# Kernel optimization log

Hardware: AMD Instinct MI355X
Metric: run time of the kernel (lower is better)

Reference implementation:

```python
import jax, jax.numpy as jnp
from jax import lax
import numpy as np

DIM = 384
HEADS = 8
B, H, W = 8, 128, 128
_DN = ('NCHW', 'OIHW', 'NCHW')


def setup_inputs() -> dict:
    key = jax.random.key(0)
    ks = jax.random.split(key, 8)
    x = jax.random.normal(ks[0], (B, DIM, H, W), jnp.float32)
    qkv_w = jax.random.normal(ks[1], (3 * DIM, DIM, 1, 1), jnp.float32) * 0.02
    qkv_b = jax.random.normal(ks[2], (3 * DIM,), jnp.float32) * 0.02
    dw_w = jax.random.normal(ks[3], (3 * DIM, 1, 3, 3), jnp.float32) * 0.02
    dw_b = jax.random.normal(ks[4], (3 * DIM,), jnp.float32) * 0.02
    proj_w = jax.random.normal(ks[5], (DIM, DIM, 1, 1), jnp.float32) * 0.02
    proj_b = jax.random.normal(ks[6], (DIM,), jnp.float32) * 0.02
    temperature = jnp.ones((HEADS, 1, 1), jnp.float32)
    return {"x": x, "qkv_w": qkv_w, "qkv_b": qkv_b, "dw_w": dw_w,
            "dw_b": dw_b, "proj_w": proj_w, "proj_b": proj_b,
            "temperature": temperature}


def _l2norm(t, eps=1e-12):
    # F.normalize(t, dim=-1): divide by max(||t||_2, eps)
    n = jnp.sqrt(jnp.sum(t * t, axis=-1, keepdims=True))
    return t / jnp.maximum(n, eps)


def reference(x, qkv_w, qkv_b, dw_w, dw_b, proj_w, proj_b, temperature):
    b, C, h, w = x.shape
    heads = HEADS
    c = C // heads
    hw = h * w
    # 1x1 pointwise qkv conv
    qkv = lax.conv_general_dilated(x, qkv_w, (1, 1), 'VALID',
                                   dimension_numbers=_DN) + qkv_b[None, :, None, None]
    # 3x3 depthwise conv, padding=1
    qkv = lax.conv_general_dilated(qkv, dw_w, (1, 1), ((1, 1), (1, 1)),
                                   feature_group_count=3 * C,
                                   dimension_numbers=_DN) + dw_b[None, :, None, None]
    q, k, v = jnp.split(qkv, 3, axis=1)
    # b (head c) h w -> b head c (h w)
    q = q.reshape(b, heads, c, hw)
    k = k.reshape(b, heads, c, hw)
    v = v.reshape(b, heads, c, hw)
    q = _l2norm(q)
    k = _l2norm(k)
    # processor scales q by temperature*sqrt(hw); SDPA divides by sqrt(hw):
    # net logits = temperature * q_n @ k_n^T  (CxC channel attention per head)
    temp = temperature.reshape(1, heads, 1, 1)
    logits = jnp.einsum('bhcn,bhdn->bhcd', q * temp, k)
    attn = jax.nn.softmax(logits, axis=-1)
    out = jnp.einsum('bhcd,bhdn->bhcn', attn, v)  # [b, heads, c, hw]
    out = out.reshape(b, C, h, w)
    return lax.conv_general_dilated(out, proj_w, (1, 1), 'VALID',
                                    dimension_numbers=_DN) + proj_b[None, :, None, None]
```

## Files before the change

### kernel.cpp

```cpp
#include <hip/hip_runtime.h>
#include <hip/hip_bf16.h>
#include <cstdint>


#define BATCH 8
#define DIM 384
#define HEADS 8
#define CH 48
#define HW 16384
#define C3 1152
#define MPAD1 1280
#define WPAD 512

typedef __attribute__((ext_vector_type(8))) short bf16x8;
typedef __attribute__((ext_vector_type(8))) unsigned short u16x8;
typedef __attribute__((ext_vector_type(4))) float f32x4;

__device__ __forceinline__ float b2f(ushort b) {
  union { float f; unsigned u; } x; x.u = ((unsigned)b) << 16; return x.f;
}
__device__ __forceinline__ ushort f2b(float f) {
  union { float f; unsigned u; } x; x.f = f;
  unsigned r = x.u + 0x7fffu + ((x.u >> 16) & 1u);
  return (ushort)(r >> 16);
}

__device__ __forceinline__ void async16(const ushort* g, ushort* l) {
  __builtin_amdgcn_global_load_lds(
      (const __attribute__((address_space(1))) unsigned int*)(unsigned long long)(uintptr_t)g,
      (__attribute__((address_space(3))) unsigned int*)(unsigned int)(uintptr_t)l,
      16, 0, 0);
}

__global__ __launch_bounds__(256) void cast_w(const float* __restrict__ s,
                                              ushort* __restrict__ d, int n) {
  int i = (blockIdx.x * 256 + threadIdx.x) * 4;
  if (i + 3 < n) {
    float4 v = *(const float4*)(s + i);
    ushort4 o = make_ushort4(f2b(v.x), f2b(v.y), f2b(v.z), f2b(v.w));
    *(ushort4*)(d + i) = o;
  }
}

template <typename SrcT, int OUT_BF16>
__global__ __launch_bounds__(512, 1) void gemm_px2(
    const ushort* __restrict__ A, const SrcT* __restrict__ src,
    const float* __restrict__ bias, void* __restrict__ Cout,
    int Mpad, int Mreal, long Asb, long Ssb, long Csb) {
  constexpr int K = DIM;
  int zb = blockIdx.y;
  int px0 = blockIdx.x * 128;
  const ushort* Ab = A + (size_t)zb * Asb;
  const SrcT* Sb = src + (size_t)zb * Ssb;
  __shared__ __align__(16) ushort Bs[128 * 384];
  __shared__ __align__(16) ushort As[2][256 * 64];
  int tid = threadIdx.x, lane = tid & 63, wid = tid >> 6;
  int wm = wid >> 1, wn = wid & 1;
  int fr = lane & 15, fs = lane >> 4;

  {
    int pix = tid & 127;
    int cg = tid >> 7;
#pragma unroll
    for (int rr = 0; rr < 12; ++rr) {
      int c8 = cg + rr * 4;
      u16x8 pk;
#pragma unroll
      for (int j = 0; j < 8; ++j) {
        int c = c8 * 8 + j;
        if constexpr (sizeof(SrcT) == 4)
          pk[j] = f2b(((const float*)Sb)[(size_t)c * HW + px0 + pix]);
        else
          pk[j] = ((const ushort*)Sb)[(size_t)c * HW + px0 + pix];
      }
      *(u16x8*)&Bs[pix * 384 + ((c8 ^ (pix & 7)) << 3)] = pk;
    }
  }

  auto stageA = [&](int buf, int mt, int k0) {
#pragma unroll
    for (int q = 0; q < 4; ++q) {
      int r = q * 64 + wid * 8 + (lane >> 3);
      int col = ((lane & 7) ^ (r & 7)) * 8;
      async16(Ab + (size_t)(mt * 256 + r) * K + k0 + col,
              &As[buf][(q * 64 + wid * 8) * 64]);
    }
  };

  f32x4 acc[4][4];
  auto compute = [&](int buf, int t) {
#pragma unroll
    for (int kk = 0; kk < 2; ++kk) {
      bf16x8 af[4], bv[4];
#pragma unroll
      for (int m = 0; m < 4; ++m) {
        int R = wm * 64 + m * 16 + fr;
        int slot = kk * 4 + fs;
        af[m] = *(const bf16x8*)&As[buf][R * 64 + ((slot ^ (R & 7)) << 3)];
      }
#pragma unroll
      for (int n = 0; n < 4; ++n) {
        int P = wn * 64 + n * 16 + fr;
        int gslot = t * 8 + kk * 4 + fs;
        bv[n] = *(const bf16x8*)&Bs[P * 384 + ((gslot ^ (P & 7)) << 3)];
      }
#pragma unroll
      for (int m = 0; m < 4; ++m)
#pragma unroll
        for (int n = 0; n < 4; ++n)
          acc[m][n] = __builtin_amdgcn_mfma_f32_16x16x32_bf16(af[m], bv[n], acc[m][n], 0, 0, 0);
    }
  };

  const int MT = Mpad >> 8;
  const int TOT = MT * 6;
  __syncthreads();
  stageA(0, 0, 0);
  stageA(1, 0, 64);
  int nmt = 0, nt = 2;

  for (int mt = 0; mt < MT; ++mt) {
    f32x4 zero = {0.f, 0.f, 0.f, 0.f};
#pragma unroll
    for (int m = 0; m < 4; ++m)
#pragma unroll
      for (int n = 0; n < 4; ++n) acc[m][n] = zero;
#pragma unroll
    for (int t = 0; t < 6; ++t) {
      int idx = mt * 6 + t;
      if (idx + 1 < TOT) {
        asm volatile("s_waitcnt vmcnt(4)" ::: "memory");
      } else {
        asm volatile("s_waitcnt vmcnt(0)" ::: "memory");
      }
      __builtin_amdgcn_s_barrier();
      asm volatile("" ::: "memory");
      __builtin_amdgcn_sched_barrier(0);
      __builtin_amdgcn_s_setprio(1);
      compute(idx & 1, t);
      __builtin_amdgcn_s_setprio(0);
      __builtin_amdgcn_sched_barrier(0);
      asm volatile("" ::: "memory");
      __builtin_amdgcn_s_barrier();
      if (idx + 2 < TOT) {
        stageA(idx & 1, nmt, nt * 64);
        if (++nt == 6) { nt = 0; ++nmt; }
      }
    }
#pragma unroll
    for (int m = 0; m < 4; ++m)
#pragma unroll
      for (int j = 0; j < 4; ++j) {
        int gr = mt * 256 + wm * 64 + m * 16 + fs * 4 + j;
        if (gr < Mreal) {
          float bz = bias[gr];
#pragma unroll
          for (int n = 0; n < 4; ++n) {
            int gc = px0 + wn * 64 + n * 16 + fr;
            float v = acc[m][n][j] + bz;
            if constexpr (OUT_BF16)
              ((ushort*)Cout)[(size_t)zb * Csb + (size_t)gr * HW + gc] = f2b(v);
            else
              ((float*)Cout)[(size_t)zb * Csb + (size_t)gr * HW + gc] = v;
          }
        }
      }
  }
}

__global__ __launch_bounds__(256) void dwconv(
    const ushort* __restrict__ in, const float* __restrict__ w9,
    const float* __restrict__ b9, ushort* __restrict__ out,
    float* __restrict__ sq) {
  int ch = blockIdx.x;
  int b = blockIdx.y;
  const size_t plane = ((size_t)b * C3 + ch) * HW;
  int tid = threadIdx.x, lane = tid & 63;
  int rg = tid >> 4, cg = tid & 15;
  int r0 = rg * 8, c0 = cg * 8;

  float w[9];
#pragma unroll
  for (int i = 0; i < 9; ++i) w[i] = w9[ch * 9 + i];
  float bias = b9[ch];

  float a0[8], a1[8];
#pragma unroll
  for (int c = 0; c < 8; ++c) { a0[c] = 0.f; a1[c] = 0.f; }
  float ss = 0.f;

#pragma unroll
  for (int it = 0; it < 10; ++it) {
    int r = r0 - 1 + it;
    float x[8];
    if ((unsigned)r < 128u) {
      u16x8 raw = *(const u16x8*)(in + plane + (size_t)r * 128 + c0);
#pragma unroll
      for (int c = 0; c < 8; ++c) x[c] = b2f(raw[c]);
    } else {
#pragma unroll
      for (int c = 0; c < 8; ++c) x[c] = 0.f;
    }
    float xl = __shfl(x[7], lane - 1);
    float xr = __shfl(x[0], lane + 1);
    if (cg == 0) xl = 0.f;
    if (cg == 15) xr = 0.f;

    float h0[8], h1[8], h2[8];
#pragma unroll
    for (int c = 0; c < 8; ++c) {
      float l = (c == 0) ? xl : x[c - 1];
      float rt = (c == 7) ? xr : x[c + 1];
      h0[c] = w[0] * l + w[1] * x[c] + w[2] * rt;
      h1[c] = w[3] * l + w[4] * x[c] + w[5] * rt;
      h2[c] = w[6] * l + w[7] * x[c] + w[8] * rt;
    }
    if (it >= 2) {
      int R = r - 1;
      u16x8 pk;
#pragma unroll
      for (int c = 0; c < 8; ++c) {
        float o = a0[c] + h2[c] + bias;
        ss += o * o;
        pk[c] = f2b(o);
      }
      *(u16x8*)(out + plane + (size_t)R * 128 + c0) = pk;
    }
#pragma unroll
    for (int c = 0; c < 8; ++c) { a0[c] = a1[c] + h1[c]; a1[c] = h0[c]; }
  }

  if (ch < 2 * DIM) {
#pragma unroll
    for (int off = 32; off; off >>= 1) ss += __shfl_down(ss, off, 64);
    if (lane == 0) atomicAdd(&sq[b * 2 * DIM + ch], ss);
  }
}

__global__ __launch_bounds__(256) void gram(const ushort* __restrict__ qkvd,
                                            float* __restrict__ G) {
  int chunk = blockIdx.x;
  int bh = blockIdx.y;
  int b = bh >> 3, h = bh & 7;
  int tid = threadIdx.x, lane = tid & 63, wid = tid >> 6;
  const ushort* qbase = qkvd + ((size_t)b * C3 + h * CH) * HW;
  const ushort* kbase = qbase + (size_t)DIM * HW;
  int pix0 = chunk * 1024 + wid * 256;
  int fr = lane & 15, fk = (lane >> 4) * 8;
  f32x4 zero = {0.f, 0.f, 0.f, 0.f};
  f32x4 acc[3][3];
#pragma unroll
  for (int i = 0; i < 3; ++i)
#pragma unroll
    for (int j = 0; j < 3; ++j) acc[i][j] = zero;
#pragma unroll
  for (int it = 0; it < 8; ++it) {
    int pix = pix0 + it * 32 + fk;
    bf16x8 aq[3], bk[3];
#pragma unroll
    for (int mi = 0; mi < 3; ++mi)
      aq[mi] = *(const bf16x8*)(qbase + (size_t)(mi * 16 + fr) * HW + pix);
#pragma unroll
    for (int ni = 0; ni < 3; ++ni)
      bk[ni] = *(const bf16x8*)(kbase + (size_t)(ni * 16 + fr) * HW + pix);
#pragma unroll
    for (int mi = 0; mi < 3; ++mi)
#pragma unroll
      for (int ni = 0; ni < 3; ++ni)
        acc[mi][ni] = __builtin_amdgcn_mfma_f32_16x16x32_bf16(aq[mi], bk[ni], acc[mi][ni], 0, 0, 0);
  }
  __shared__ float gs[CH * CH];
  for (int i = tid; i < CH * CH; i += 256) gs[i] = 0.f;
  __syncthreads();
  int crow = (lane >> 4) * 4, ccol = lane & 15;
#pragma unroll
  for (int mi = 0; mi < 3; ++mi)
#pragma unroll
    for (int ni = 0; ni < 3; ++ni)
#pragma unroll
      for (int j = 0; j < 4; ++j)
        atomicAdd(&gs[(mi * 16 + crow + j) * CH + ni * 16 + ccol], acc[mi][ni][j]);
  __syncthreads();
  float* Gp = G + (size_t)bh * CH * CH;
  for (int i = tid; i < CH * CH; i += 256) atomicAdd(&Gp[i], gs[i]);
}

__global__ void softmax_k(const float* __restrict__ G, const float* __restrict__ sq,
                          const float* __restrict__ temp, float* __restrict__ attn) {
  int bh = blockIdx.x, b = bh >> 3, h = bh & 7;
  int lane = threadIdx.x;
  __shared__ float inq[CH], ink[CH];
  if (lane < CH) {
    inq[lane] = 1.f / fmaxf(sqrtf(sq[b * 2 * DIM + h * CH + lane]), 1e-12f);
    ink[lane] = 1.f / fmaxf(sqrtf(sq[b * 2 * DIM + DIM + h * CH + lane]), 1e-12f);
  }
  __syncthreads();
  if (lane < CH) {
    float t = temp[h] * inq[lane];
    const float* g = G + (size_t)bh * CH * CH + lane * CH;
    float v[CH];
    float mx = -1e30f;
#pragma unroll
    for (int d = 0; d < CH; ++d) { v[d] = t * g[d] * ink[d]; mx = fmaxf(mx, v[d]); }
    float s = 0.f;
#pragma unroll
    for (int d = 0; d < CH; ++d) { v[d] = expf(v[d] - mx); s += v[d]; }
    float inv = 1.f / s;
    float* a = attn + (size_t)bh * CH * CH + lane * CH;
#pragma unroll
    for (int d = 0; d < CH; ++d) a[d] = v[d] * inv;
  }
}

__global__ __launch_bounds__(384) void weff_k(const float* __restrict__ pw,
                                              const float* __restrict__ attn,
                                              ushort* __restrict__ weff) {
  int dg = threadIdx.x;
  int p = blockIdx.x;
  int b = blockIdx.y;
  int h = dg / CH, d = dg - h * CH;
  const float* a = attn + (((size_t)b * HEADS + h) * CH) * CH + d;
  const float* wrow = pw + (size_t)p * DIM + h * CH;
  float s = 0.f;
#pragma unroll
  for (int c = 0; c < CH; ++c) s += wrow[c] * a[c * CH];
  weff[((size_t)b * WPAD + p) * DIM + dg] = f2b(s);
}

extern "C" void kernel_launch(void* const* d_in, const int* in_sizes, int n_in,
                              void* d_out, int out_size, void* d_ws, size_t ws_size,
                              hipStream_t stream) {
  const float* x = (const float*)d_in[0];
  const float* qkv_w = (const float*)d_in[1];
  const float* qkv_b = (const float*)d_in[2];
  const float* dw_w = (const float*)d_in[3];
  const float* dw_b = (const float*)d_in[4];
  const float* proj_w = (const float*)d_in[5];
  const float* proj_b = (const float*)d_in[6];
  const float* temp = (const float*)d_in[7];

  const size_t SZ_C1 = (size_t)BATCH * C3 * HW * 2;
  const size_t SZ_WQB = (size_t)MPAD1 * DIM * 2;
  const size_t SZ_SQ = (size_t)BATCH * 2 * DIM * 4;
  const size_t SZ_G = (size_t)BATCH * HEADS * CH * CH * 4;
  const size_t SZ_WEFF = (size_t)BATCH * WPAD * DIM * 2;

  const size_t OFF_C1 = 0;
  const size_t OFF_QKVD = OFF_C1 + SZ_C1;
  const size_t OFF_WQB = OFF_QKVD + SZ_C1;
  const size_t OFF_SQ = OFF_WQB + SZ_WQB;
  const size_t OFF_G = OFF_SQ + SZ_SQ;
  const size_t OFF_ATTN = OFF_G + SZ_G;
  const size_t OFF_WEFF = OFF_ATTN + SZ_G;
  const size_t TOTAL = OFF_WEFF + SZ_WEFF;
  if (ws_size < TOTAL) return;

  char* ws = (char*)d_ws;
  ushort* c1 = (ushort*)(ws + OFF_C1);
  ushort* qkvd = (ushort*)(ws + OFF_QKVD);
  ushort* wqb = (ushort*)(ws + OFF_WQB);
  float* sq = (float*)(ws + OFF_SQ);
  float* G = (float*)(ws + OFF_G);
  float* attn = (float*)(ws + OFF_ATTN);
  ushort* weff = (ushort*)(ws + OFF_WEFF);

  hipMemsetAsync(ws + OFF_SQ, 0, SZ_SQ + SZ_G, stream);

  cast_w<<<(C3 * DIM) / 1024, 256, 0, stream>>>(qkv_w, wqb, C3 * DIM);
  gemm_px2<float, 1><<<dim3(HW / 128, BATCH), 512, 0, stream>>>(
      wqb, x, qkv_b, (void*)c1, MPAD1, C3, 0L, (long)DIM * HW, (long)C3 * HW);
  dwconv<<<dim3(C3, BATCH), 256, 0, stream>>>(c1, dw_w, dw_b, qkvd, sq);
  gram<<<dim3(16, BATCH * HEADS), 256, 0, stream>>>(qkvd, G);
  softmax_k<<<BATCH * HEADS, 64, 0, stream>>>(G, sq, temp, attn);
  weff_k<<<dim3(DIM, BATCH), 384, 0, stream>>>(proj_w, attn, weff);
  gemm_px2<ushort, 0><<<dim3(HW / 128, BATCH), 512, 0, stream>>>(
      weff, qkvd + (size_t)2 * DIM * HW, proj_b, d_out, WPAD, DIM,
      (long)WPAD * DIM, (long)C3 * HW, (long)DIM * HW);
}
```

Measured before the change: 601.6 us.

## Stage GEMM epilogue through LDS for coalesced vector stores

The GEMM epilogue now writes accumulators plus bias into shared memory (reusing the A staging buffer), then stores full 16-byte vectors per thread to global memory in row-contiguous chunks, instead of scattered 2- or 4-byte stores. Because the A buffer is reused for output staging, cross-tile prefetch of the next M tile's A slices is removed: the next tile's first two stages are issued only after the epilogue finishes. The intent is to remove uncoalesced write traffic in exchange for extra barriers and lost overlap at tile boundaries.

```diff
diff --git a/kernel.cpp b/kernel.cpp
--- a/kernel.cpp
+++ b/kernel.cpp
@@ -113,11 +113,9 @@
   };
 
   const int MT = Mpad >> 8;
-  const int TOT = MT * 6;
   __syncthreads();
   stageA(0, 0, 0);
   stageA(1, 0, 64);
-  int nmt = 0, nt = 2;
 
   for (int mt = 0; mt < MT; ++mt) {
     f32x4 zero = {0.f, 0.f, 0.f, 0.f};
@@ -125,47 +123,84 @@
     for (int m = 0; m < 4; ++m)
 #pragma unroll
       for (int n = 0; n < 4; ++n) acc[m][n] = zero;
+
 #pragma unroll
     for (int t = 0; t < 6; ++t) {
-      int idx = mt * 6 + t;
-      if (idx + 1 < TOT) {
+      if (t < 5) {
         asm volatile("s_waitcnt vmcnt(4)" ::: "memory");
       } else {
         asm volatile("s_waitcnt vmcnt(0)" ::: "memory");
       }
       __builtin_amdgcn_s_barrier();
-      asm volatile("" ::: "memory");
-      __builtin_amdgcn_sched_barrier(0);
       __builtin_amdgcn_s_setprio(1);
-      compute(idx & 1, t);
+      compute(t & 1, t);
       __builtin_amdgcn_s_setprio(0);
-      __builtin_amdgcn_sched_barrier(0);
-      asm volatile("" ::: "memory");
       __builtin_amdgcn_s_barrier();
-      if (idx + 2 < TOT) {
-        stageA(idx & 1, nmt, nt * 64);
-        if (++nt == 6) { nt = 0; ++nmt; }
-      }
-    }
-#pragma unroll
-    for (int m = 0; m < 4; ++m)
-#pragma unroll
-      for (int j = 0; j < 4; ++j) {
-        int gr = mt * 256 + wm * 64 + m * 16 + fs * 4 + j;
-        if (gr < Mreal) {
-          float bz = bias[gr];
-#pragma unroll
-          for (int n = 0; n < 4; ++n) {
-            int gc = px0 + wn * 64 + n * 16 + fr;
-            float v = acc[m][n][j] + bz;
-            if constexpr (OUT_BF16)
-              ((ushort*)Cout)[(size_t)zb * Csb + (size_t)gr * HW + gc] = f2b(v);
-            else
-              ((float*)Cout)[(size_t)zb * Csb + (size_t)gr * HW + gc] = v;
-          }
+      if (t < 4) stageA(t & 1, mt, (t + 2) * 64);
+    }
+
+    if constexpr (OUT_BF16) {
+      ushort* Cs = &As[0][0];
+#pragma unroll
+      for (int m = 0; m < 4; ++m)
+#pragma unroll
+        for (int j = 0; j < 4; ++j) {
+          int R = wm * 64 + m * 16 + fs * 4 + j;
+          int gr = mt * 256 + R;
+          float bz = (gr < Mreal) ? bias[gr] : 0.f;
+#pragma unroll
+          for (int n = 0; n < 4; ++n)
+            Cs[R * 128 + wn * 64 + n * 16 + fr] = f2b(acc[m][n][j] + bz);
         }
-      }
-  }
+      __syncthreads();
+#pragma unroll
+      for (int it = 0; it < 8; ++it) {
+        int chunk = it * 512 + tid;
+        int row = chunk >> 4, c16 = chunk & 15;
+        int gr = mt * 256 + row;
+        if (gr < Mreal)
+          *(u16x8*)((ushort*)Cout + (size_t)zb * Csb + (size_t)gr * HW + px0 + c16 * 8) =
+              *(const u16x8*)&Cs[row * 128 + c16 * 8];
+      }
+      __syncthreads();
+    } else {
+      float* Cf = (float*)&As[0][0];
+#pragma unroll
+      for (int p = 0; p < 2; ++p) {
+        if ((wm >> 1) == p) {
+          int Rb = (wm & 1) * 64;
+#pragma unroll
+          for (int m = 0; m < 4; ++m)
+#pragma unroll
+            for (int j = 0; j < 4; ++j) {
+              int R = Rb + m * 16 + fs * 4 + j;
+              int gr = mt * 256 + p * 128 + R;
+              float bz = (gr < Mreal) ? bias[gr] : 0.f;
+#pragma unroll
+              for (int n = 0; n < 4; ++n)
+                Cf[R * 128 + wn * 64 + n * 16 + fr] = acc[m][n][j] + bz;
+            }
+        }
+        __syncthreads();
+#pragma unroll
+        for (int it = 0; it < 8; ++it) {
+          int chunk = it * 512 + tid;
+          int row = chunk >> 5, c4 = chunk & 31;
+          int gr = mt * 256 + p * 128 + row;
+          if (gr < Mreal)
+            *(float4*)((float*)Cout + (size_t)zb * Csb + (size_t)gr * HW + px0 + c4 * 4) =
+                *(const float4*)&Cf[row * 128 + c4 * 4];
+        }
+        __syncthreads();
+      }
+    }
+
+    if (mt + 1 < MT) {
+      stageA(0, mt + 1, 0);
+      stageA(1, mt + 1, 64);
+    }
+  }
+  asm volatile("s_waitcnt vmcnt(0)" ::: "memory");
 }
 
 __global__ __launch_bounds__(256) void dwconv(
```

After: 613.0 us. No clear change (+1.9%).
